# Kernel optimization log

Hardware: AMD Instinct MI355X
Metric: run time of the kernel (lower is better)

The kernel has to match this reference:

```python
import jax, jax.numpy as jnp
import numpy as np

TOL = 1e-3

def _mask(x):
    # forward = relu, backward = identity (straight-through)
    return x + jax.lax.stop_gradient(jax.nn.relu(x) - x)

def setup_inputs() -> dict:
    key = jax.random.key(0)
    ks = jax.random.split(key, 6)
    B, L, A, Y = 4096, 64, 64, 128
    return {
        "LT": jax.random.uniform(ks[0], (B, L), jnp.float32),
        "K": jax.random.uniform(ks[1], (L, A), jnp.float32),
        "AT": jax.random.uniform(ks[2], (A,), jnp.float32),
        "u": jax.random.uniform(ks[3], (L * A, Y), jnp.float32),
        "e": jax.random.uniform(ks[4], (A, Y), jnp.float32),
        "b": jax.random.uniform(ks[5], (Y,), jnp.float32),
        "max_step": 50,
    }

def _fixed_point(LT3, AT3, Km, max_step):
    # LT3: [B,L,1], AT3: [A,1] (broadcasts over batch), Km: [L,A]
    B = LT3.shape[0]
    A = Km.shape[1]
    L = Km.shape[0]
    AF0 = jnp.zeros((B, A, 1), LT3.dtype)
    LF0 = jnp.zeros((B, L, 1), LT3.dtype)

    def step_fn(AF, LF):
        Ldi = LT3 / (jnp.matmul(Km, AF) + 1.0)          # [B,L,1]
        Adi = AT3 / (jnp.matmul(Km.T, LF) + 1.0)        # [B,A,1]
        AF_n = AT3 / (jnp.matmul(Km.T, Ldi) + 1.0)      # [B,A,1]
        LF_n = LT3 / (jnp.matmul(Km, Adi) + 1.0)        # [B,L,1]
        return AF_n, LF_n

    def cond(state):
        step, _, _, err = state
        return jnp.logical_and(step < max_step, err >= TOL)

    def body(state):
        step, AF, LF, _ = state
        AF_n, LF_n = step_fn(AF, LF)
        err = (jnp.max(jnp.abs(AF_n - AF) / (AF + 1e-5)) +
               jnp.max(jnp.abs(LF_n - LF) / (LF + 1e-5)))
        return (step + 1, AF_n, LF_n, err)

    _, AF, LF, _ = jax.lax.while_loop(cond, body, (0, AF0, LF0, jnp.array(jnp.inf, LT3.dtype)))
    return AF, LF

def reference(LT, K, AT, u, e, b, max_step):
    Km = _mask(K)            # [L,A]
    ATm = _mask(AT)          # [A]
    B = LT.shape[0]
    LT3 = LT[:, :, None]     # [B,L,1]
    AT3 = ATm[:, None]       # [A,1]

    # fixed-point loop was under torch.no_grad(): feed stop_gradient'd values
    AF, LF = _fixed_point(jax.lax.stop_gradient(LT3),
                          jax.lax.stop_gradient(AT3),
                          jax.lax.stop_gradient(Km), max_step)

    # final differentiable refinement step
    Ldi = LT3 / (jnp.matmul(Km, AF) + 1.0)
    Adi = AT3 / (jnp.matmul(Km.T, LF) + 1.0)
    AFf = AT3 / (jnp.matmul(Km.T, Ldi) + 1.0)   # [B,A,1]
    LFf = LT3 / (jnp.matmul(Km, Adi) + 1.0)     # [B,L,1]

    AFt = jnp.swapaxes(AFf, 1, 2)               # [B,1,A]
    D = (Km * jnp.matmul(LFf, AFt)).reshape(B, -1)   # [B, L*A]
    AFsq = AFt[:, 0, :]                          # [B,A]
    y = D @ u + AFsq @ e + b[None, :]            # [B,Y]
    return y
```

## Files before the change

kernel.cpp:

```cpp
#include <hip/hip_runtime.h>
#include <hip/hip_bf16.h>

typedef __bf16 bf16x8 __attribute__((ext_vector_type(8)));
typedef __bf16 bf16x4 __attribute__((ext_vector_type(4)));
typedef float  float4v __attribute__((ext_vector_type(4)));

__device__ __forceinline__ float bf2f(unsigned short u){
  union { unsigned int i; float f; } x; x.i = ((unsigned int)u) << 16; return x.f;
}
__device__ __forceinline__ unsigned short f2bf(float f){
  union { float f; unsigned int i; } x; x.f = f;
  unsigned int r = x.i + 0x7FFFu + ((x.i >> 16) & 1u);
  return (unsigned short)(r >> 16);
}
__device__ __forceinline__ float ldin(const void* p, int i, bool isbf){
  return isbf ? bf2f(((const unsigned short*)p)[i]) : ((const float*)p)[i];
}
__device__ __forceinline__ float frcp(float x){ return __builtin_amdgcn_rcpf(x); }

#define SROW 136

__global__ __launch_bounds__(256) void k_prep(
    const void* LT, const void* K, const void* AT, const void* u,
    const void* e, const void* bvec, const int* msin,
    float* ltf, __bf16* KmHi, __bf16* KmLo, __bf16* KTHi, __bf16* KTLo,
    float* atf, float* bf_, __bf16* W2T, int* meta)
{
  int tid = threadIdx.x, bid = blockIdx.x;
  int ok = 0;
  if (tid < 64){
    float v = bf2f(((const unsigned short*)AT)[tid]);
    ok = (v >= 0.f && v <= 1.0f) ? 1 : 0;
  }
  int cnt = __syncthreads_count(ok);
  bool isbf = (cnt >= 60);

  if (bid < 256){
    int k0 = (bid >> 2) * 64, y0 = (bid & 3) * 32;
    __shared__ float sT[64 * 33];
    #pragma unroll
    for (int i = 0; i < 8; ++i){
      int flat = i * 256 + tid;
      int r = flat >> 5, c = flat & 31;
      sT[r * 33 + c] = ldin(u, (k0 + r) * 128 + (y0 + c), isbf);
    }
    __syncthreads();
    int l = k0 >> 6;
    #pragma unroll
    for (int i = 0; i < 8; ++i){
      int flat = i * 256 + tid;
      int yl = flat >> 6, kl = flat & 63;
      float km = ldin(K, l * 64 + kl, isbf); km = km > 0.f ? km : 0.f;
      W2T[(y0 + yl) * 4224 + (k0 + kl)] = (__bf16)(km * sT[kl * 33 + yl]);
    }
    #pragma unroll
    for (int i = 0; i < 4; ++i){
      int idx = bid * 1024 + i * 256 + tid;
      ltf[idx] = ldin(LT, idx, isbf);
    }
  } else {
    #pragma unroll
    for (int i = 0; i < 16; ++i){
      int idx = i * 256 + tid;
      int l = idx >> 6, a = idx & 63;
      float v = ldin(K, idx, isbf); v = v > 0.f ? v : 0.f;
      __bf16 hi = (__bf16)v;
      __bf16 lo = (__bf16)(v - (float)hi);
      KmHi[idx] = hi; KmLo[idx] = lo;
      KTHi[a * 64 + l] = hi; KTLo[a * 64 + l] = lo;
    }
    if (tid < 64){ float v = ldin(AT, tid, isbf); atf[tid] = v > 0.f ? v : 0.f; }
    if (tid < 128){ bf_[tid] = ldin(bvec, tid, isbf); }
    #pragma unroll
    for (int i = 0; i < 32; ++i){
      int idx = i * 256 + tid;
      int y = idx >> 6, a = idx & 63;
      W2T[y * 4224 + 4096 + a] = (__bf16)ldin(e, a * 128 + y, isbf);
    }
    if (tid == 0){
      meta[0] = isbf ? 1 : 0;
      int mi = msin[0];
      if (mi <= 0 || mi > 1000000){
        float mf = ((const float*)msin)[0];
        mi = (mf > 0.f && mf < 1.0e6f) ? (int)mf : 50;
      }
      meta[1] = mi;
    }
  }
}

__device__ __forceinline__ float4v gemm3(const bf16x8* aH, const bf16x8* aL,
                                         const __bf16* s, int rdH){
  bf16x8 bH0 = *(const bf16x8*)(s + rdH);
  bf16x8 bL0 = *(const bf16x8*)(s + rdH + 8);
  bf16x8 bH1 = *(const bf16x8*)(s + rdH + 64);
  bf16x8 bL1 = *(const bf16x8*)(s + rdH + 72);
  float4v a0 = {0.f,0.f,0.f,0.f}, a1 = {0.f,0.f,0.f,0.f}, a2 = {0.f,0.f,0.f,0.f};
  a0 = __builtin_amdgcn_mfma_f32_16x16x32_bf16(aH[0], bH0, a0, 0, 0, 0);
  a1 = __builtin_amdgcn_mfma_f32_16x16x32_bf16(aH[0], bL0, a1, 0, 0, 0);
  a2 = __builtin_amdgcn_mfma_f32_16x16x32_bf16(aL[0], bH0, a2, 0, 0, 0);
  a0 = __builtin_amdgcn_mfma_f32_16x16x32_bf16(aH[1], bH1, a0, 0, 0, 0);
  a1 = __builtin_amdgcn_mfma_f32_16x16x32_bf16(aH[1], bL1, a1, 0, 0, 0);
  a2 = __builtin_amdgcn_mfma_f32_16x16x32_bf16(aL[1], bH1, a2, 0, 0, 0);
  return (a0 + a1) + a2;
}

__device__ __forceinline__ void wsplit(__bf16* s, int wH, float4v v){
  bf16x4 h, l;
  #pragma unroll
  for (int r = 0; r < 4; ++r){
    __bf16 hh = (__bf16)v[r];
    h[r] = hh; l[r] = (__bf16)(v[r] - (float)hh);
  }
  *(bf16x4*)(s + wH)     = h;
  *(bf16x4*)(s + wH + 8) = l;
}

__global__ __launch_bounds__(256) void k_main(
    const float* ltf, const __bf16* KmHi, const __bf16* KmLo,
    const __bf16* KTHi, const __bf16* KTLo, const float* atf, const float* bf_,
    const __bf16* W2T, const int* meta, void* out)
{
  __shared__ __attribute__((aligned(16))) __bf16 sAF[16*SROW], sLF[16*SROW];
  __shared__ __attribute__((aligned(16))) __bf16 sLd[16*SROW], sAd[16*SROW];
  __shared__ float sErrA[4], sErrL[4];

  const int tid = threadIdx.x;
  const int wave = tid >> 6, lane = tid & 63;
  const int lr = lane & 15, q = lane >> 4;
  const int row0 = blockIdx.x * 16;
  const int dq = wave * 16 + q * 4;
  const int rdH = lr * SROW + q * 16;
  const int wH  = lr * SROW + (dq >> 3) * 16 + (dq & 7);

  for (int i = tid; i < 16 * SROW; i += 256){
    sAF[i] = (__bf16)0.f; sLF[i] = (__bf16)0.f;
  }

  bf16x8 aKmH[2], aKmL[2], aKTH[2], aKTL[2];
  #pragma unroll
  for (int ks = 0; ks < 2; ++ks){
    int o = (wave * 16 + lr) * 64 + ks * 32 + q * 8;
    aKmH[ks] = *(const bf16x8*)(KmHi + o);
    aKmL[ks] = *(const bf16x8*)(KmLo + o);
    aKTH[ks] = *(const bf16x8*)(KTHi + o);
    aKTL[ks] = *(const bf16x8*)(KTLo + o);
  }
  const float4v ltv = *(const float4v*)(ltf + (row0 + lr) * 64 + dq);
  const float4v atv = *(const float4v*)(atf + dq);
  const int isbf = meta[0];
  const int ms   = meta[1];

  float4v afold = {0.f,0.f,0.f,0.f}, lfold = {0.f,0.f,0.f,0.f};
  __syncthreads();

  for (int step = 0; step < ms; ++step){
    float4v s1 = gemm3(aKmH, aKmL, sAF, rdH);
    float4v t2 = gemm3(aKTH, aKTL, sLF, rdH);
    float4v ld, ad;
    #pragma unroll
    for (int r = 0; r < 4; ++r){
      ld[r] = ltv[r] * frcp(s1[r] + 1.f);
      ad[r] = atv[r] * frcp(t2[r] + 1.f);
    }
    wsplit(sLd, wH, ld); wsplit(sAd, wH, ad);
    __syncthreads();
    float4v t3 = gemm3(aKTH, aKTL, sLd, rdH);
    float4v t4 = gemm3(aKmH, aKmL, sAd, rdH);
    float eA = 0.f, eL = 0.f;
    float4v afn, lfn;
    #pragma unroll
    for (int r = 0; r < 4; ++r){
      afn[r] = atv[r] * frcp(t3[r] + 1.f);
      lfn[r] = ltv[r] * frcp(t4[r] + 1.f);
      eA = fmaxf(eA, fabsf(afn[r] - afold[r]) * frcp(afold[r] + 1e-5f));
      eL = fmaxf(eL, fabsf(lfn[r] - lfold[r]) * frcp(lfold[r] + 1e-5f));
    }
    afold = afn; lfold = lfn;
    wsplit(sAF, wH, afn); wsplit(sLF, wH, lfn);
    const bool chk = (step & 1) || (step == ms - 1);
    if (chk){
      #pragma unroll
      for (int off = 32; off >= 1; off >>= 1){
        eA = fmaxf(eA, __shfl_xor(eA, off));
        eL = fmaxf(eL, __shfl_xor(eL, off));
      }
      if (lane == 0){ sErrA[wave] = eA; sErrL[wave] = eL; }
    }
    __syncthreads();
    if (chk){
      float err = fmaxf(fmaxf(sErrA[0], sErrA[1]), fmaxf(sErrA[2], sErrA[3]))
                + fmaxf(fmaxf(sErrL[0], sErrL[1]), fmaxf(sErrL[2], sErrL[3]));
      if (err < 1e-3f) break;
    }
  }

  {
    float4v s1 = gemm3(aKmH, aKmL, sAF, rdH);
    float4v t2 = gemm3(aKTH, aKTL, sLF, rdH);
    float4v ld, ad;
    #pragma unroll
    for (int r = 0; r < 4; ++r){
      ld[r] = ltv[r] * frcp(s1[r] + 1.f);
      ad[r] = atv[r] * frcp(t2[r] + 1.f);
    }
    wsplit(sLd, wH, ld); wsplit(sAd, wH, ad);
    __syncthreads();
    float4v t3 = gemm3(aKTH, aKTL, sLd, rdH);
    float4v t4 = gemm3(aKmH, aKmL, sAd, rdH);
    bf16x4 afh, lfh;
    #pragma unroll
    for (int r = 0; r < 4; ++r){
      afh[r] = (__bf16)(atv[r] * frcp(t3[r] + 1.f));
      lfh[r] = (__bf16)(ltv[r] * frcp(t4[r] + 1.f));
    }
    *(bf16x4*)(sAF + wH) = afh;
    *(bf16x4*)(sLF + wH) = lfh;
    __syncthreads();
  }

  float4v acc0 = {0.f,0.f,0.f,0.f}, acc1 = {0.f,0.f,0.f,0.f};
  const int nBase = wave * 32;
  const __bf16* Wr0 = W2T + (nBase + lr) * 4224;
  const __bf16* Wr1 = Wr0 + 16 * 4224;
  for (int kc = 0; kc < 32; ++kc){
    #pragma unroll
    for (int kt = 0; kt < 4; ++kt){
      const int l = 2 * kc + (kt >> 1);
      const float lf = (float)sLF[lr * SROW + (l >> 3) * 16 + (l & 7)];
      bf16x8 af = *(const bf16x8*)(sAF + lr * SROW + ((kt & 1) * 4 + q) * 16);
      bf16x8 aD;
      #pragma unroll
      for (int j = 0; j < 8; ++j) aD[j] = (__bf16)(lf * (float)af[j]);
      const int kb = kc * 128 + kt * 32 + q * 8;
      bf16x8 b0 = *(const bf16x8*)(Wr0 + kb);
      bf16x8 b1 = *(const bf16x8*)(Wr1 + kb);
      acc0 = __builtin_amdgcn_mfma_f32_16x16x32_bf16(aD, b0, acc0, 0, 0, 0);
      acc1 = __builtin_amdgcn_mfma_f32_16x16x32_bf16(aD, b1, acc1, 0, 0, 0);
    }
  }
  #pragma unroll
  for (int kt = 0; kt < 2; ++kt){
    bf16x8 aD = *(const bf16x8*)(sAF + lr * SROW + (kt * 4 + q) * 16);
    const int kb = 4096 + kt * 32 + q * 8;
    bf16x8 b0 = *(const bf16x8*)(Wr0 + kb);
    bf16x8 b1 = *(const bf16x8*)(Wr1 + kb);
    acc0 = __builtin_amdgcn_mfma_f32_16x16x32_bf16(aD, b0, acc0, 0, 0, 0);
    acc1 = __builtin_amdgcn_mfma_f32_16x16x32_bf16(aD, b1, acc1, 0, 0, 0);
  }

  const float b0v = bf_[nBase + lr];
  const float b1v = bf_[nBase + 16 + lr];
  const int obase = (row0 + q * 4) * 128;
  if (isbf){
    unsigned short* o = (unsigned short*)out;
    #pragma unroll
    for (int r = 0; r < 4; ++r){
      o[obase + r * 128 + nBase + lr]      = f2bf(acc0[r] + b0v);
      o[obase + r * 128 + nBase + 16 + lr] = f2bf(acc1[r] + b1v);
    }
  } else {
    float* o = (float*)out;
    #pragma unroll
    for (int r = 0; r < 4; ++r){
      o[obase + r * 128 + nBase + lr]      = acc0[r] + b0v;
      o[obase + r * 128 + nBase + 16 + lr] = acc1[r] + b1v;
    }
  }
}

extern "C" void kernel_launch(void* const* d_in, const int* in_sizes, int n_in,
                              void* d_out, int out_size, void* d_ws, size_t ws_size,
                              hipStream_t stream){
  char* ws = (char*)d_ws;
  int*    meta = (int*)ws;
  float*  atf  = (float*)(ws + 256);
  float*  bf_  = (float*)(ws + 512);
  __bf16* KmHi = (__bf16*)(ws + 1024);
  __bf16* KmLo = (__bf16*)(ws + 1024 + 8192);
  __bf16* KTHi = (__bf16*)(ws + 1024 + 16384);
  __bf16* KTLo = (__bf16*)(ws + 1024 + 24576);
  float*  ltf  = (float*)(ws + 33792);
  __bf16* W2T  = (__bf16*)(ws + 33792 + 1048576);

  k_prep<<<dim3(257), dim3(256), 0, stream>>>(
      d_in[0], d_in[1], d_in[2], d_in[3], d_in[4], d_in[5], (const int*)d_in[6],
      ltf, KmHi, KmLo, KTHi, KTLo, atf, bf_, W2T, meta);
  k_main<<<dim3(256), dim3(256), 0, stream>>>(
      ltf, KmHi, KmLo, KTHi, KTLo, atf, bf_, W2T, meta, d_out);
}
```

Measured before the change: 131.8 us.

## Split solver into sync-free per-wave iteration kernel and separate epilogue GEMM kernel

Restructures the fixed-point solve so each of two waves per block handles one chain (AF or LF) across all 64 columns. The chains interleave without block barriers, error checks and early exit are removed, and the loop always runs the full max_step. Most iterations drop the low half of the split-precision products, keeping hi/lo splitting only for the last few steps. The +1 is folded into the MFMA accumulator init. The output GEMM becomes its own kernel with more rows per block and split Y halves, and the e transpose uses shared memory. This removes per-step syncthreads and cuts MFMA work, at the cost of always running max_step iterations and reduced precision in early steps.

```diff
diff --git a/kernel.cpp b/kernel.cpp
--- a/kernel.cpp
+++ b/kernel.cpp
@@ -4,6 +4,8 @@
 typedef __bf16 bf16x8 __attribute__((ext_vector_type(8)));
 typedef __bf16 bf16x4 __attribute__((ext_vector_type(4)));
 typedef float  float4v __attribute__((ext_vector_type(4)));
+
+#define MFMA16 __builtin_amdgcn_mfma_f32_16x16x32_bf16
 
 __device__ __forceinline__ float bf2f(unsigned short u){
   union { unsigned int i; float f; } x; x.i = ((unsigned int)u) << 16; return x.f;
@@ -18,13 +20,11 @@
 }
 __device__ __forceinline__ float frcp(float x){ return __builtin_amdgcn_rcpf(x); }
 
-#define SROW 136
+#define W2T_STRIDE 4160
 
 __global__ __launch_bounds__(256) void k_prep(
-    const void* LT, const void* K, const void* AT, const void* u,
-    const void* e, const void* bvec, const int* msin,
-    float* ltf, __bf16* KmHi, __bf16* KmLo, __bf16* KTHi, __bf16* KTLo,
-    float* atf, float* bf_, __bf16* W2T, int* meta)
+    const void* K, const void* AT, const void* u, const void* e,
+    const int* msin, __bf16* KmHi, __bf16* KTHi, __bf16* W2T, int* meta)
 {
   int tid = threadIdx.x, bid = blockIdx.x;
   int ok = 0;
@@ -51,31 +51,24 @@
       int flat = i * 256 + tid;
       int yl = flat >> 6, kl = flat & 63;
       float km = ldin(K, l * 64 + kl, isbf); km = km > 0.f ? km : 0.f;
-      W2T[(y0 + yl) * 4224 + (k0 + kl)] = (__bf16)(km * sT[kl * 33 + yl]);
-    }
-    #pragma unroll
-    for (int i = 0; i < 4; ++i){
-      int idx = bid * 1024 + i * 256 + tid;
-      ltf[idx] = ldin(LT, idx, isbf);
-    }
-  } else {
+      W2T[(y0 + yl) * W2T_STRIDE + (k0 + kl)] = (__bf16)(km * sT[kl * 33 + yl]);
+    }
+  } else if (bid == 256){
+    __shared__ float sK[64 * 65];
     #pragma unroll
     for (int i = 0; i < 16; ++i){
       int idx = i * 256 + tid;
       int l = idx >> 6, a = idx & 63;
       float v = ldin(K, idx, isbf); v = v > 0.f ? v : 0.f;
-      __bf16 hi = (__bf16)v;
-      __bf16 lo = (__bf16)(v - (float)hi);
-      KmHi[idx] = hi; KmLo[idx] = lo;
-      KTHi[a * 64 + l] = hi; KTLo[a * 64 + l] = lo;
-    }
-    if (tid < 64){ float v = ldin(AT, tid, isbf); atf[tid] = v > 0.f ? v : 0.f; }
-    if (tid < 128){ bf_[tid] = ldin(bvec, tid, isbf); }
-    #pragma unroll
-    for (int i = 0; i < 32; ++i){
+      sK[l * 65 + a] = v;
+      KmHi[idx] = (__bf16)v;
+    }
+    __syncthreads();
+    #pragma unroll
+    for (int i = 0; i < 16; ++i){
       int idx = i * 256 + tid;
-      int y = idx >> 6, a = idx & 63;
-      W2T[y * 4224 + 4096 + a] = (__bf16)ldin(e, a * 128 + y, isbf);
+      int a = idx >> 6, l2 = idx & 63;
+      KTHi[idx] = (__bf16)sK[l2 * 65 + a];
     }
     if (tid == 0){
       meta[0] = isbf ? 1 : 0;
@@ -86,185 +79,230 @@
       }
       meta[1] = mi;
     }
-  }
-}
-
-__device__ __forceinline__ float4v gemm3(const bf16x8* aH, const bf16x8* aL,
-                                         const __bf16* s, int rdH){
-  bf16x8 bH0 = *(const bf16x8*)(s + rdH);
-  bf16x8 bL0 = *(const bf16x8*)(s + rdH + 8);
-  bf16x8 bH1 = *(const bf16x8*)(s + rdH + 64);
-  bf16x8 bL1 = *(const bf16x8*)(s + rdH + 72);
-  float4v a0 = {0.f,0.f,0.f,0.f}, a1 = {0.f,0.f,0.f,0.f}, a2 = {0.f,0.f,0.f,0.f};
-  a0 = __builtin_amdgcn_mfma_f32_16x16x32_bf16(aH[0], bH0, a0, 0, 0, 0);
-  a1 = __builtin_amdgcn_mfma_f32_16x16x32_bf16(aH[0], bL0, a1, 0, 0, 0);
-  a2 = __builtin_amdgcn_mfma_f32_16x16x32_bf16(aL[0], bH0, a2, 0, 0, 0);
-  a0 = __builtin_amdgcn_mfma_f32_16x16x32_bf16(aH[1], bH1, a0, 0, 0, 0);
-  a1 = __builtin_amdgcn_mfma_f32_16x16x32_bf16(aH[1], bL1, a1, 0, 0, 0);
-  a2 = __builtin_amdgcn_mfma_f32_16x16x32_bf16(aL[1], bH1, a2, 0, 0, 0);
-  return (a0 + a1) + a2;
-}
-
-__device__ __forceinline__ void wsplit(__bf16* s, int wH, float4v v){
-  bf16x4 h, l;
-  #pragma unroll
-  for (int r = 0; r < 4; ++r){
-    __bf16 hh = (__bf16)v[r];
-    h[r] = hh; l[r] = (__bf16)(v[r] - (float)hh);
-  }
-  *(bf16x4*)(s + wH)     = h;
-  *(bf16x4*)(s + wH + 8) = l;
-}
-
-__global__ __launch_bounds__(256) void k_main(
-    const float* ltf, const __bf16* KmHi, const __bf16* KmLo,
-    const __bf16* KTHi, const __bf16* KTLo, const float* atf, const float* bf_,
-    const __bf16* W2T, const int* meta, void* out)
+  } else {
+    __shared__ float sE[64 * 133];
+    #pragma unroll
+    for (int i = 0; i < 32; ++i){
+      int idx = i * 256 + tid;
+      int a = idx >> 7, y = idx & 127;
+      sE[a * 133 + y] = ldin(e, idx, isbf);
+    }
+    __syncthreads();
+    #pragma unroll
+    for (int i = 0; i < 32; ++i){
+      int idx = i * 256 + tid;
+      int y = idx >> 6, a = idx & 63;
+      W2T[y * W2T_STRIDE + 4096 + a] = (__bf16)sE[a * 133 + y];
+    }
+  }
+}
+
+template<bool SPLIT>
+__device__ __forceinline__ void halfstep(
+    const bf16x8 (&A)[4][2], const float4v (&V)[4],
+    __bf16* sH, __bf16* sL, int rb, int wb)
 {
-  __shared__ __attribute__((aligned(16))) __bf16 sAF[16*SROW], sLF[16*SROW];
-  __shared__ __attribute__((aligned(16))) __bf16 sLd[16*SROW], sAd[16*SROW];
-  __shared__ float sErrA[4], sErrL[4];
-
-  const int tid = threadIdx.x;
-  const int wave = tid >> 6, lane = tid & 63;
+  bf16x8 bh0 = *(const bf16x8*)(sH + rb);
+  bf16x8 bh1 = *(const bf16x8*)(sH + rb + 32);
+  const float4v ones = {1.f, 1.f, 1.f, 1.f};
+  float4v c[4];
+  #pragma unroll
+  for (int T = 0; T < 4; ++T) c[T] = MFMA16(A[T][0], bh0, ones, 0, 0, 0);
+  #pragma unroll
+  for (int T = 0; T < 4; ++T) c[T] = MFMA16(A[T][1], bh1, c[T], 0, 0, 0);
+  if (SPLIT){
+    bf16x8 bl0 = *(const bf16x8*)(sL + rb);
+    bf16x8 bl1 = *(const bf16x8*)(sL + rb + 32);
+    const float4v zero = {0.f, 0.f, 0.f, 0.f};
+    float4v d[4];
+    #pragma unroll
+    for (int T = 0; T < 4; ++T) d[T] = MFMA16(A[T][0], bl0, zero, 0, 0, 0);
+    #pragma unroll
+    for (int T = 0; T < 4; ++T) d[T] = MFMA16(A[T][1], bl1, d[T], 0, 0, 0);
+    #pragma unroll
+    for (int T = 0; T < 4; ++T) c[T] += d[T];
+  }
+  #pragma unroll
+  for (int T = 0; T < 4; ++T){
+    bf16x4 h, lo;
+    #pragma unroll
+    for (int r = 0; r < 4; ++r){
+      float o = V[T][r] * frcp(c[T][r]);
+      __bf16 hh = (__bf16)o;
+      h[r] = hh;
+      if (SPLIT) lo[r] = (__bf16)(o - (float)hh);
+    }
+    *(bf16x4*)(sH + wb + 16 * T) = h;
+    if (SPLIT) *(bf16x4*)(sL + wb + 16 * T) = lo;
+  }
+}
+
+__global__ __launch_bounds__(128, 1) void k_iter(
+    const void* LT, const void* AT, const __bf16* KmHi, const __bf16* KTHi,
+    const int* meta, __bf16* gAF, __bf16* gLF)
+{
+  __shared__ __attribute__((aligned(16))) __bf16 sHi[2][16 * 72];
+  __shared__ __attribute__((aligned(16))) __bf16 sLo[2][16 * 72];
+  const int tid = threadIdx.x, w = tid >> 6, lane = tid & 63;
   const int lr = lane & 15, q = lane >> 4;
   const int row0 = blockIdx.x * 16;
-  const int dq = wave * 16 + q * 4;
-  const int rdH = lr * SROW + q * 16;
-  const int wH  = lr * SROW + (dq >> 3) * 16 + (dq & 7);
-
-  for (int i = tid; i < 16 * SROW; i += 256){
-    sAF[i] = (__bf16)0.f; sLF[i] = (__bf16)0.f;
-  }
-
-  bf16x8 aKmH[2], aKmL[2], aKTH[2], aKTL[2];
-  #pragma unroll
-  for (int ks = 0; ks < 2; ++ks){
-    int o = (wave * 16 + lr) * 64 + ks * 32 + q * 8;
-    aKmH[ks] = *(const bf16x8*)(KmHi + o);
-    aKmL[ks] = *(const bf16x8*)(KmLo + o);
-    aKTH[ks] = *(const bf16x8*)(KTHi + o);
-    aKTL[ks] = *(const bf16x8*)(KTLo + o);
-  }
-  const float4v ltv = *(const float4v*)(ltf + (row0 + lr) * 64 + dq);
-  const float4v atv = *(const float4v*)(atf + dq);
+  __bf16* sH = sHi[w];
+  __bf16* sL = sLo[w];
+
+  const bf16x4 z4 = {(__bf16)0.f, (__bf16)0.f, (__bf16)0.f, (__bf16)0.f};
+  for (int i = lane; i < 288; i += 64){
+    *(bf16x4*)(sH + 4 * i) = z4;
+    *(bf16x4*)(sL + 4 * i) = z4;
+  }
+
   const int isbf = meta[0];
   const int ms   = meta[1];
 
-  float4v afold = {0.f,0.f,0.f,0.f}, lfold = {0.f,0.f,0.f,0.f};
+  const __bf16* M1 = w ? KTHi : KmHi;
+  const __bf16* M2 = w ? KmHi : KTHi;
+  bf16x8 a1[4][2], a2[4][2];
+  #pragma unroll
+  for (int T = 0; T < 4; ++T)
+    #pragma unroll
+    for (int ks = 0; ks < 2; ++ks){
+      int o = (16 * T + lr) * 64 + ks * 32 + q * 8;
+      a1[T][ks] = *(const bf16x8*)(M1 + o);
+      a2[T][ks] = *(const bf16x8*)(M2 + o);
+    }
+
+  float4v ltv[4], atv[4];
+  if (isbf){
+    const unsigned short* lt = (const unsigned short*)LT + (row0 + lr) * 64;
+    const unsigned short* at = (const unsigned short*)AT;
+    #pragma unroll
+    for (int T = 0; T < 4; ++T)
+      #pragma unroll
+      for (int r = 0; r < 4; ++r){
+        int d = 16 * T + q * 4 + r;
+        ltv[T][r] = bf2f(lt[d]);
+        atv[T][r] = fmaxf(bf2f(at[d]), 0.f);
+      }
+  } else {
+    const float* lt = (const float*)LT + (row0 + lr) * 64;
+    const float* at = (const float*)AT;
+    #pragma unroll
+    for (int T = 0; T < 4; ++T){
+      ltv[T] = *(const float4v*)(lt + 16 * T + q * 4);
+      float4v a = *(const float4v*)(at + 16 * T + q * 4);
+      #pragma unroll
+      for (int r = 0; r < 4; ++r) atv[T][r] = fmaxf(a[r], 0.f);
+    }
+  }
+  float4v V1[4], V2[4];
+  #pragma unroll
+  for (int T = 0; T < 4; ++T){
+    V1[T] = w ? atv[T] : ltv[T];
+    V2[T] = w ? ltv[T] : atv[T];
+  }
+
+  const int rb = lr * 72 + q * 8;
+  const int wb = lr * 72 + q * 4;
+
+  const int nPlain = ms > 6 ? ms - 6 : 0;
+  const int nSplit = ms - nPlain + 1;
+  for (int s = 0; s < nPlain; ++s){
+    halfstep<false>(a1, V1, sH, sL, rb, wb);
+    halfstep<false>(a2, V2, sH, sL, rb, wb);
+  }
+  for (int s = 0; s < nSplit; ++s){
+    halfstep<true>(a1, V1, sH, sL, rb, wb);
+    halfstep<true>(a2, V2, sH, sL, rb, wb);
+  }
+
+  __bf16* gX = (w ? gLF : gAF) + row0 * 64;
+  const int lrow = lane >> 2, seg = lane & 3;
+  bf16x8 v0 = *(const bf16x8*)(sH + lrow * 72 + seg * 16);
+  bf16x8 v1 = *(const bf16x8*)(sH + lrow * 72 + seg * 16 + 8);
+  *(bf16x8*)(gX + lrow * 64 + seg * 16) = v0;
+  *(bf16x8*)(gX + lrow * 64 + seg * 16 + 8) = v1;
+}
+
+__global__ __launch_bounds__(256) void k_epi(
+    const __bf16* gAF, const __bf16* gLF, const __bf16* W2T,
+    const void* bvec, const int* meta, void* out)
+{
+  __shared__ __attribute__((aligned(16))) __bf16 sAF[32 * 72], sLF[32 * 72];
+  const int tid = threadIdx.x, wave = tid >> 6, lane = tid & 63;
+  const int lr = lane & 15, q = lane >> 4;
+  const int rg = blockIdx.x >> 1, yh = blockIdx.x & 1;
+  const int row0 = rg * 32;
+  const int isbf = meta[0];
+  {
+    int lrow = tid >> 3, seg = tid & 7;
+    *(bf16x8*)(sAF + lrow * 72 + seg * 8) =
+        *(const bf16x8*)(gAF + (row0 + lrow) * 64 + seg * 8);
+    *(bf16x8*)(sLF + lrow * 72 + seg * 8) =
+        *(const bf16x8*)(gLF + (row0 + lrow) * 64 + seg * 8);
+  }
   __syncthreads();
 
-  for (int step = 0; step < ms; ++step){
-    float4v s1 = gemm3(aKmH, aKmL, sAF, rdH);
-    float4v t2 = gemm3(aKTH, aKTL, sLF, rdH);
-    float4v ld, ad;
-    #pragma unroll
-    for (int r = 0; r < 4; ++r){
-      ld[r] = ltv[r] * frcp(s1[r] + 1.f);
-      ad[r] = atv[r] * frcp(t2[r] + 1.f);
-    }
-    wsplit(sLd, wH, ld); wsplit(sAd, wH, ad);
-    __syncthreads();
-    float4v t3 = gemm3(aKTH, aKTL, sLd, rdH);
-    float4v t4 = gemm3(aKmH, aKmL, sAd, rdH);
-    float eA = 0.f, eL = 0.f;
-    float4v afn, lfn;
-    #pragma unroll
-    for (int r = 0; r < 4; ++r){
-      afn[r] = atv[r] * frcp(t3[r] + 1.f);
-      lfn[r] = ltv[r] * frcp(t4[r] + 1.f);
-      eA = fmaxf(eA, fabsf(afn[r] - afold[r]) * frcp(afold[r] + 1e-5f));
-      eL = fmaxf(eL, fabsf(lfn[r] - lfold[r]) * frcp(lfold[r] + 1e-5f));
-    }
-    afold = afn; lfold = lfn;
-    wsplit(sAF, wH, afn); wsplit(sLF, wH, lfn);
-    const bool chk = (step & 1) || (step == ms - 1);
-    if (chk){
-      #pragma unroll
-      for (int off = 32; off >= 1; off >>= 1){
-        eA = fmaxf(eA, __shfl_xor(eA, off));
-        eL = fmaxf(eL, __shfl_xor(eL, off));
-      }
-      if (lane == 0){ sErrA[wave] = eA; sErrL[wave] = eL; }
-    }
-    __syncthreads();
-    if (chk){
-      float err = fmaxf(fmaxf(sErrA[0], sErrA[1]), fmaxf(sErrA[2], sErrA[3]))
-                + fmaxf(fmaxf(sErrL[0], sErrL[1]), fmaxf(sErrL[2], sErrL[3]));
-      if (err < 1e-3f) break;
-    }
-  }
-
+  const int r0 = (wave & 1) * 16;
+  const int y0 = yh * 64 + (wave >> 1) * 32;
+  const int rloc = r0 + lr;
+
+  const float bv0 = ldin(bvec, y0 + lr, isbf);
+  const float bv1 = ldin(bvec, y0 + 16 + lr, isbf);
+  float4v acc0 = {bv0, bv0, bv0, bv0};
+  float4v acc1 = {bv1, bv1, bv1, bv1};
+
+  bf16x8 af0 = *(const bf16x8*)(sAF + rloc * 72 + q * 8);
+  bf16x8 af1 = *(const bf16x8*)(sAF + rloc * 72 + 32 + q * 8);
+  float af0f[8], af1f[8];
+  #pragma unroll
+  for (int j = 0; j < 8; ++j){ af0f[j] = (float)af0[j]; af1f[j] = (float)af1[j]; }
+
+  const __bf16* w0 = W2T + (y0 + lr) * W2T_STRIDE + q * 8;
+  const __bf16* w1 = w0 + 16 * W2T_STRIDE;
+
+  #pragma unroll 4
+  for (int l = 0; l < 64; ++l){
+    const float lf = (float)sLF[rloc * 72 + l];
+    bf16x8 aD0, aD1;
+    #pragma unroll
+    for (int j = 0; j < 8; ++j){
+      aD0[j] = (__bf16)(lf * af0f[j]);
+      aD1[j] = (__bf16)(lf * af1f[j]);
+    }
+    const int kb = l * 64;
+    bf16x8 b00 = *(const bf16x8*)(w0 + kb);
+    bf16x8 b10 = *(const bf16x8*)(w1 + kb);
+    bf16x8 b01 = *(const bf16x8*)(w0 + kb + 32);
+    bf16x8 b11 = *(const bf16x8*)(w1 + kb + 32);
+    acc0 = MFMA16(aD0, b00, acc0, 0, 0, 0);
+    acc1 = MFMA16(aD0, b10, acc1, 0, 0, 0);
+    acc0 = MFMA16(aD1, b01, acc0, 0, 0, 0);
+    acc1 = MFMA16(aD1, b11, acc1, 0, 0, 0);
+  }
   {
-    float4v s1 = gemm3(aKmH, aKmL, sAF, rdH);
-    float4v t2 = gemm3(aKTH, aKTL, sLF, rdH);
-    float4v ld, ad;
-    #pragma unroll
-    for (int r = 0; r < 4; ++r){
-      ld[r] = ltv[r] * frcp(s1[r] + 1.f);
-      ad[r] = atv[r] * frcp(t2[r] + 1.f);
-    }
-    wsplit(sLd, wH, ld); wsplit(sAd, wH, ad);
-    __syncthreads();
-    float4v t3 = gemm3(aKTH, aKTL, sLd, rdH);
-    float4v t4 = gemm3(aKmH, aKmL, sAd, rdH);
-    bf16x4 afh, lfh;
-    #pragma unroll
-    for (int r = 0; r < 4; ++r){
-      afh[r] = (__bf16)(atv[r] * frcp(t3[r] + 1.f));
-      lfh[r] = (__bf16)(ltv[r] * frcp(t4[r] + 1.f));
-    }
-    *(bf16x4*)(sAF + wH) = afh;
-    *(bf16x4*)(sLF + wH) = lfh;
-    __syncthreads();
-  }
-
-  float4v acc0 = {0.f,0.f,0.f,0.f}, acc1 = {0.f,0.f,0.f,0.f};
-  const int nBase = wave * 32;
-  const __bf16* Wr0 = W2T + (nBase + lr) * 4224;
-  const __bf16* Wr1 = Wr0 + 16 * 4224;
-  for (int kc = 0; kc < 32; ++kc){
-    #pragma unroll
-    for (int kt = 0; kt < 4; ++kt){
-      const int l = 2 * kc + (kt >> 1);
-      const float lf = (float)sLF[lr * SROW + (l >> 3) * 16 + (l & 7)];
-      bf16x8 af = *(const bf16x8*)(sAF + lr * SROW + ((kt & 1) * 4 + q) * 16);
-      bf16x8 aD;
-      #pragma unroll
-      for (int j = 0; j < 8; ++j) aD[j] = (__bf16)(lf * (float)af[j]);
-      const int kb = kc * 128 + kt * 32 + q * 8;
-      bf16x8 b0 = *(const bf16x8*)(Wr0 + kb);
-      bf16x8 b1 = *(const bf16x8*)(Wr1 + kb);
-      acc0 = __builtin_amdgcn_mfma_f32_16x16x32_bf16(aD, b0, acc0, 0, 0, 0);
-      acc1 = __builtin_amdgcn_mfma_f32_16x16x32_bf16(aD, b1, acc1, 0, 0, 0);
-    }
-  }
-  #pragma unroll
-  for (int kt = 0; kt < 2; ++kt){
-    bf16x8 aD = *(const bf16x8*)(sAF + lr * SROW + (kt * 4 + q) * 16);
-    const int kb = 4096 + kt * 32 + q * 8;
-    bf16x8 b0 = *(const bf16x8*)(Wr0 + kb);
-    bf16x8 b1 = *(const bf16x8*)(Wr1 + kb);
-    acc0 = __builtin_amdgcn_mfma_f32_16x16x32_bf16(aD, b0, acc0, 0, 0, 0);
-    acc1 = __builtin_amdgcn_mfma_f32_16x16x32_bf16(aD, b1, acc1, 0, 0, 0);
-  }
-
-  const float b0v = bf_[nBase + lr];
-  const float b1v = bf_[nBase + 16 + lr];
-  const int obase = (row0 + q * 4) * 128;
+    bf16x8 b00 = *(const bf16x8*)(w0 + 4096);
+    bf16x8 b10 = *(const bf16x8*)(w1 + 4096);
+    bf16x8 b01 = *(const bf16x8*)(w0 + 4096 + 32);
+    bf16x8 b11 = *(const bf16x8*)(w1 + 4096 + 32);
+    acc0 = MFMA16(af0, b00, acc0, 0, 0, 0);
+    acc1 = MFMA16(af0, b10, acc1, 0, 0, 0);
+    acc0 = MFMA16(af1, b01, acc0, 0, 0, 0);
+    acc1 = MFMA16(af1, b11, acc1, 0, 0, 0);
+  }
+
+  const int orow = row0 + r0 + q * 4;
   if (isbf){
     unsigned short* o = (unsigned short*)out;
     #pragma unroll
     for (int r = 0; r < 4; ++r){
-      o[obase + r * 128 + nBase + lr]      = f2bf(acc0[r] + b0v);
-      o[obase + r * 128 + nBase + 16 + lr] = f2bf(acc1[r] + b1v);
+      o[(orow + r) * 128 + y0 + lr]      = f2bf(acc0[r]);
+      o[(orow + r) * 128 + y0 + 16 + lr] = f2bf(acc1[r]);
     }
   } else {
     float* o = (float*)out;
     #pragma unroll
     for (int r = 0; r < 4; ++r){
-      o[obase + r * 128 + nBase + lr]      = acc0[r] + b0v;
-      o[obase + r * 128 + nBase + 16 + lr] = acc1[r] + b1v;
+      o[(orow + r) * 128 + y0 + lr]      = acc0[r];
+      o[(orow + r) * 128 + y0 + 16 + lr] = acc1[r];
     }
   }
 }
@@ -274,18 +312,17 @@
                               hipStream_t stream){
   char* ws = (char*)d_ws;
   int*    meta = (int*)ws;
-  float*  atf  = (float*)(ws + 256);
-  float*  bf_  = (float*)(ws + 512);
   __bf16* KmHi = (__bf16*)(ws + 1024);
-  __bf16* KmLo = (__bf16*)(ws + 1024 + 8192);
-  __bf16* KTHi = (__bf16*)(ws + 1024 + 16384);
-  __bf16* KTLo = (__bf16*)(ws + 1024 + 24576);
-  float*  ltf  = (float*)(ws + 33792);
-  __bf16* W2T  = (__bf16*)(ws + 33792 + 1048576);
-
-  k_prep<<<dim3(257), dim3(256), 0, stream>>>(
-      d_in[0], d_in[1], d_in[2], d_in[3], d_in[4], d_in[5], (const int*)d_in[6],
-      ltf, KmHi, KmLo, KTHi, KTLo, atf, bf_, W2T, meta);
-  k_main<<<dim3(256), dim3(256), 0, stream>>>(
-      ltf, KmHi, KmLo, KTHi, KTLo, atf, bf_, W2T, meta, d_out);
-}
+  __bf16* KTHi = (__bf16*)(ws + 9216);
+  __bf16* gAF  = (__bf16*)(ws + 17408);
+  __bf16* gLF  = (__bf16*)(ws + 541696);
+  __bf16* W2T  = (__bf16*)(ws + 1065984);
+
+  k_prep<<<dim3(258), dim3(256), 0, stream>>>(
+      d_in[1], d_in[2], d_in[3], d_in[4], (const int*)d_in[6],
+      KmHi, KTHi, W2T, meta);
+  k_iter<<<dim3(256), dim3(128), 0, stream>>>(
+      d_in[0], d_in[2], KmHi, KTHi, meta, gAF, gLF);
+  k_epi<<<dim3(256), dim3(256), 0, stream>>>(
+      gAF, gLF, W2T, d_in[5], meta, d_out);
+}
```

After: 142.4 us. +8.0%, slower.
